# Optimization experiments

Hardware: AMD Instinct MI355X
Metric: run time of the kernel (lower is better)

## Reference

```python
import jax, jax.numpy as jnp
import numpy as np

B = 8192
LOD = 60      # latent_obs_dim
LSD = 2 * LOD # latent state dim
AD = 10       # act_dim
NB = 15       # num_basis
BW = 3        # bandwidth
H = 60        # control-net hidden units


def elup1(x):
    # exp(x) if x < 0 else x + 1 (positive covariance activation)
    return jnp.where(x < 0.0, jnp.exp(x), x + 1.0)


def setup_inputs() -> dict:
    key = jax.random.key(0)
    ks = jax.random.split(key, 16)
    inp = {
        "post_mean": jax.random.normal(ks[0], (B, LSD), jnp.float32),
        "cu": jax.random.uniform(ks[1], (B, LOD), jnp.float32) + 0.1,
        "cl": jax.random.uniform(ks[2], (B, LOD), jnp.float32) + 0.1,
        "cs": 0.01 * jax.random.normal(ks[3], (B, LOD), jnp.float32),
        "action": jax.random.normal(ks[4], (B, AD), jnp.float32),
        # transition basis matrices (params); original init is zeros/+-0.2*I,
        # use small random values for a non-degenerate numerical test
        "tm11": 0.05 * jax.random.normal(ks[5], (NB, LOD, LOD), jnp.float32),
        "tm12": 0.2 * jnp.eye(LOD)[None] + 0.02 * jax.random.normal(ks[6], (NB, LOD, LOD), jnp.float32),
        "tm21": -0.2 * jnp.eye(LOD)[None] + 0.02 * jax.random.normal(ks[7], (NB, LOD, LOD), jnp.float32),
        "tm22": 0.05 * jax.random.normal(ks[8], (NB, LOD, LOD), jnp.float32),
        # log transition noise, init elup1_inv(1.0) = 0.0 -> perturb slightly
        "log_noise": 0.1 * jax.random.normal(ks[9], (1, LSD), jnp.float32),
        # coefficient net: Linear(LSD -> NB) + Softmax (no hidden layers)
        "w_coef": jax.random.normal(ks[10], (NB, LSD), jnp.float32) / np.sqrt(LSD),
        "b_coef": jnp.zeros((NB,), jnp.float32),
        # control net: Linear(AD -> H) + ReLU + Linear(H -> LSD)
        "w_c1": jax.random.normal(ks[11], (H, AD), jnp.float32) / np.sqrt(AD),
        "b_c1": jnp.zeros((H,), jnp.float32),
        "w_c2": jax.random.normal(ks[12], (LSD, H), jnp.float32) / np.sqrt(H),
        "b_c2": jnp.zeros((LSD,), jnp.float32),
    }
    return inp


def _band_mask():
    idx = jnp.arange(LOD)
    return (jnp.abs(idx[:, None] - idx[None, :]) <= BW).astype(jnp.float32)


def reference(post_mean, cu, cl, cs, action,
              tm11, tm12, tm21, tm22, log_noise,
              w_coef, b_coef, w_c1, b_c1, w_c2, b_c2):
    mask = _band_mask()            # [LOD, LOD]
    eye = jnp.eye(LOD, dtype=post_mean.dtype)

    # coefficient net + softmax -> basis-weighted transition matrices
    coef = jax.nn.softmax(post_mean @ w_coef.T + b_coef, axis=-1)  # [B, NB]

    def mix(tm):  # [B, LOD, LOD], band-masked
        return jnp.einsum('bk,kij->bij', coef, tm) * mask

    t11 = mix(tm11) + eye
    t12 = mix(tm12)
    t21 = mix(tm21)
    t22 = mix(tm22) + eye

    # control net contribution
    control = jax.nn.relu(action @ w_c1.T + b_c1) @ w_c2.T + b_c2  # [B, LSD]

    trans_cov = elup1(log_noise)        # [1, LSD]
    tc_u = trans_cov[..., :LOD]
    tc_l = trans_cov[..., LOD:]

    mu = post_mean[:, :LOD]
    ml = post_mean[:, LOD:]

    bmv = lambda m, v: jnp.einsum('bij,bj->bi', m, v)

    nmu = bmv(t11, mu) + bmv(t12, ml)
    nml = bmv(t21, mu) + bmv(t22, ml)

    # diagonal covariance predict (dadat / dadbt)
    ncu = bmv(t11 ** 2, cu) + 2.0 * bmv(t11 * t12, cs) + bmv(t12 ** 2, cl) + tc_u
    ncl = bmv(t21 ** 2, cu) + 2.0 * bmv(t21 * t22, cs) + bmv(t22 ** 2, cl) + tc_l
    ncs = bmv(t21 * t11, cu) + bmv(t22 * t11, cs) + bmv(t21 * t12, cs) + bmv(t22 * t12, cl)

    next_mean = jnp.concatenate([nmu, nml], axis=-1) + control
    return (next_mean, ncu, ncl, ncs)
```

## Files before the change

### kernel.cpp

```cpp
#include <hip/hip_runtime.h>
#include <math.h>

#define BATCH 8192
#define LOD 60
#define LSD 120
#define AD 10
#define NB 15
#define BW 3
#define H 60

#define NM_SZ (BATCH * LSD)
#define NC_SZ (BATCH * LOD)

#define RGS 6
#define RG_ROWS 10
#define NJJ 16
#define VSJ 65
#define VSV (NJJ * VSJ)
#define VS_FLOATS (5 * VSV)
#define PACK_FLOATS (RG_ROWS * NB * 28)
#define OST_PLANE (RG_ROWS * 65)
#define OVL2 (VS_FLOATS + PACK_FLOATS)

__device__ __forceinline__ float elup1f(float x) {
    return x < 0.0f ? __expf(x) : x + 1.0f;
}

__global__ __launch_bounds__(256, 3) void k_fused(
    const float* __restrict__ pm, const float* __restrict__ cu,
    const float* __restrict__ cl, const float* __restrict__ cs,
    const float* __restrict__ action,
    const float* __restrict__ tm11, const float* __restrict__ tm12,
    const float* __restrict__ tm21, const float* __restrict__ tm22,
    const float* __restrict__ log_noise,
    const float* __restrict__ w_coef, const float* __restrict__ b_coef,
    const float* __restrict__ w_c1, const float* __restrict__ b_c1,
    const float* __restrict__ w_c2, const float* __restrict__ b_c2,
    float* __restrict__ out)
{
    __shared__ float coef_s[NB * 64];
    __shared__ __align__(16) float ovl[OVL2];

    const int tid  = threadIdx.x;
    const int wave = tid >> 6;
    const int lane = tid & 63;
    const int wv   = __builtin_amdgcn_readfirstlane(wave);

    const int bid  = blockIdx.x;
    const int xcd  = bid & 7;
    const int slot = bid >> 3;
    const int bg   = xcd * 16 + slot / RGS;
    const int rg   = slot % RGS;
    const int b0   = bg * 64;
    const int i0   = rg * RG_ROWS;

    {
        const int k0 = wv, k1 = wv + 4, k2 = wv + 8;
        const int k3 = (wv < 3) ? wv + 12 : 14;
        const float4* pmv = (const float4*)(pm + (size_t)(b0 + lane) * LSD);
        const float4* w0 = (const float4*)(w_coef + k0 * LSD);
        const float4* w1 = (const float4*)(w_coef + k1 * LSD);
        const float4* w2 = (const float4*)(w_coef + k2 * LSD);
        const float4* w3 = (const float4*)(w_coef + k3 * LSD);
        float a0 = b_coef[k0], a1 = b_coef[k1], a2 = b_coef[k2], a3 = b_coef[k3];
        #pragma unroll 6
        for (int d = 0; d < LSD / 4; ++d) {
            float4 p = pmv[d];
            float4 u0 = w0[d], u1 = w1[d], u2 = w2[d], u3 = w3[d];
            a0 = fmaf(p.x, u0.x, a0); a0 = fmaf(p.y, u0.y, a0);
            a0 = fmaf(p.z, u0.z, a0); a0 = fmaf(p.w, u0.w, a0);
            a1 = fmaf(p.x, u1.x, a1); a1 = fmaf(p.y, u1.y, a1);
            a1 = fmaf(p.z, u1.z, a1); a1 = fmaf(p.w, u1.w, a1);
            a2 = fmaf(p.x, u2.x, a2); a2 = fmaf(p.y, u2.y, a2);
            a2 = fmaf(p.z, u2.z, a2); a2 = fmaf(p.w, u2.w, a2);
            a3 = fmaf(p.x, u3.x, a3); a3 = fmaf(p.y, u3.y, a3);
            a3 = fmaf(p.z, u3.z, a3); a3 = fmaf(p.w, u3.w, a3);
        }
        coef_s[k0 * 64 + lane] = a0;
        coef_s[k1 * 64 + lane] = a1;
        coef_s[k2 * 64 + lane] = a2;
        if (wv < 3) coef_s[k3 * 64 + lane] = a3;
    }
    __syncthreads();

    float* vsb    = ovl;
    float* pack_s = ovl + VS_FLOATS;

    for (int idx = tid; idx < 5 * 64 * NJJ; idx += 256) {
        int jj  = idx & 15;
        int blc = (idx >> 4) & 63;
        int v   = idx >> 10;
        int j   = i0 - BW + jj;
        int bb  = b0 + blc;
        float val = 0.0f;
        if (j >= 0 && j < LOD) {
            if (v == 0)      val = pm[bb * LSD + j];
            else if (v == 1) val = pm[bb * LSD + LOD + j];
            else if (v == 2) val = cu[bb * LOD + j];
            else if (v == 3) val = cl[bb * LOD + j];
            else             val = cs[bb * LOD + j];
        }
        vsb[v * VSV + jj * VSJ + blc] = val;
    }
    for (int idx = tid; idx < PACK_FLOATS; idx += 256) {
        int m  = idx & 3;
        int q  = idx >> 2;
        int jo = q % 7;
        int q2 = q / 7;
        int k  = q2 % NB;
        int ri = q2 / NB;
        int i  = i0 + ri;
        int j  = i - BW + jo;
        const float* tmm = (m == 0) ? tm11 : (m == 1) ? tm12 : (m == 2) ? tm21 : tm22;
        float val = (j >= 0 && j < LOD) ? tmm[k * (LOD * LOD) + i * LOD + j] : 0.0f;
        pack_s[idx] = val;
    }

    if (tid < 64) {
        float v[NB];
        float mx = -1e30f;
        #pragma unroll
        for (int k = 0; k < NB; ++k) { v[k] = coef_s[k * 64 + tid]; mx = fmaxf(mx, v[k]); }
        float sm = 0.0f;
        #pragma unroll
        for (int k = 0; k < NB; ++k) { v[k] = __expf(v[k] - mx); sm += v[k]; }
        float inv = 1.0f / sm;
        #pragma unroll
        for (int k = 0; k < NB; ++k) coef_s[k * 64 + tid] = v[k] * inv;
    }

    const int lim   = (wv < 2) ? 2 : 1;
    const int rbase = (wv < 2) ? wv * 3 : 6 + (wv - 2) * 2;
    int rcl[3];
    rcl[0] = rbase; rcl[1] = rbase + 1; rcl[2] = rbase + lim;

    float ctl[6];
    #pragma unroll
    for (int rr = 0; rr < 3; ++rr) {
        ctl[rr]     = b_c2[i0 + rcl[rr]];
        ctl[3 + rr] = b_c2[LOD + i0 + rcl[rr]];
    }
    {
        float av[AD];
        const float2* a2p = (const float2*)(action + (size_t)(b0 + lane) * AD);
        #pragma unroll
        for (int z = 0; z < 5; ++z) { float2 t2 = a2p[z]; av[2 * z] = t2.x; av[2 * z + 1] = t2.y; }
        #pragma unroll 4
        for (int h = 0; h < H; ++h) {
            float hv = b_c1[h];
            #pragma unroll
            for (int a = 0; a < AD; ++a) hv = fmaf(av[a], w_c1[h * AD + a], hv);
            hv = fmaxf(hv, 0.0f);
            #pragma unroll
            for (int rr = 0; rr < 3; ++rr) {
                ctl[rr]     = fmaf(hv, w_c2[(i0 + rcl[rr]) * H + h], ctl[rr]);
                ctl[3 + rr] = fmaf(hv, w_c2[(LOD + i0 + rcl[rr]) * H + h], ctl[3 + rr]);
            }
        }
    }
    __syncthreads();

    float cf[NB];
    #pragma unroll
    for (int k = 0; k < NB; ++k) cf[k] = coef_s[k * 64 + lane];

    float onm[3], onl[3], ouv[3], olv[3], osv[3];
    #pragma unroll
    for (int rr = 0; rr < 3; ++rr) {
        const int riu = rcl[rr];
        const int iu  = i0 + riu;

        float t[28];
        #pragma unroll
        for (int z = 0; z < 28; ++z) t[z] = 0.0f;
        const float4* tp = (const float4*)pack_s + riu * (NB * 7);
        #pragma unroll
        for (int k = 0; k < NB; ++k) {
            float c = cf[k];
            #pragma unroll
            for (int jo = 0; jo < 7; ++jo) {
                float4 tv = tp[k * 7 + jo];
                t[jo * 4 + 0] = fmaf(c, tv.x, t[jo * 4 + 0]);
                t[jo * 4 + 1] = fmaf(c, tv.y, t[jo * 4 + 1]);
                t[jo * 4 + 2] = fmaf(c, tv.z, t[jo * 4 + 2]);
                t[jo * 4 + 3] = fmaf(c, tv.w, t[jo * 4 + 3]);
            }
        }
        t[3 * 4 + 0] += 1.0f;
        t[3 * 4 + 3] += 1.0f;

        float nmu = 0.f, nml = 0.f, ncuv = 0.f, nclv = 0.f, ncsv = 0.f;
        #pragma unroll
        for (int jo = 0; jo < 7; ++jo) {
            const int jj = riu + jo;
            float m_ = vsb[0 * VSV + jj * VSJ + lane];
            float n_ = vsb[1 * VSV + jj * VSJ + lane];
            float u_ = vsb[2 * VSV + jj * VSJ + lane];
            float l_ = vsb[3 * VSV + jj * VSJ + lane];
            float s_ = vsb[4 * VSV + jj * VSJ + lane];
            float A = t[jo * 4 + 0], Bv = t[jo * 4 + 1];
            float C = t[jo * 4 + 2], D  = t[jo * 4 + 3];
            nmu = fmaf(A, m_, nmu);  nmu = fmaf(Bv, n_, nmu);
            nml = fmaf(C, m_, nml);  nml = fmaf(D, n_, nml);
            float e1 = fmaf(Bv, s_, A * u_);
            float e2 = fmaf(Bv, l_, A * s_);
            float f1 = fmaf(D, s_, C * u_);
            float f2 = fmaf(D, l_, C * s_);
            ncuv = fmaf(A, e1, ncuv);  ncuv = fmaf(Bv, e2, ncuv);
            nclv = fmaf(C, f1, nclv);  nclv = fmaf(D, f2, nclv);
            ncsv = fmaf(C, e1, ncsv);  ncsv = fmaf(D, e2, ncsv);
        }
        ncuv += elup1f(log_noise[iu]);
        nclv += elup1f(log_noise[LOD + iu]);
        nmu  += ctl[rr];
        nml  += ctl[3 + rr];
        onm[rr] = nmu; onl[rr] = nml; ouv[rr] = ncuv; olv[rr] = nclv; osv[rr] = ncsv;
    }
    __syncthreads();

    float* ost = ovl + VS_FLOATS;
    #pragma unroll
    for (int rr = 0; rr < 3; ++rr) {
        const int ri = rcl[rr];
        ost[0 * OST_PLANE + ri * 65 + lane] = onm[rr];
        ost[1 * OST_PLANE + ri * 65 + lane] = onl[rr];
        ost[2 * OST_PLANE + ri * 65 + lane] = ouv[rr];
        ost[3 * OST_PLANE + ri * 65 + lane] = olv[rr];
        ost[4 * OST_PLANE + ri * 65 + lane] = osv[rr];
    }
    __syncthreads();

    for (int idx = tid; idx < 5 * 64 * 16; idx += 256) {
        int rq  = idx & 15;
        if (rq >= RG_ROWS) continue;
        int blc = (idx >> 4) & 63;
        int t5  = idx >> 10;
        int bb  = b0 + blc;
        float v = ost[t5 * OST_PLANE + rq * 65 + blc];
        float* bp;
        if (t5 == 0)      bp = out + bb * LSD + i0;
        else if (t5 == 1) bp = out + bb * LSD + LOD + i0;
        else if (t5 == 2) bp = out + NM_SZ + bb * LOD + i0;
        else if (t5 == 3) bp = out + NM_SZ + NC_SZ + bb * LOD + i0;
        else              bp = out + NM_SZ + 2 * NC_SZ + bb * LOD + i0;
        bp[rq] = v;
    }
}

extern "C" void kernel_launch(void* const* d_in, const int* in_sizes, int n_in,
                              void* d_out, int out_size, void* d_ws, size_t ws_size,
                              hipStream_t stream) {
    (void)in_sizes; (void)n_in; (void)out_size; (void)d_ws; (void)ws_size;
    const float* pm        = (const float*)d_in[0];
    const float* cu        = (const float*)d_in[1];
    const float* cl        = (const float*)d_in[2];
    const float* cs        = (const float*)d_in[3];
    const float* action    = (const float*)d_in[4];
    const float* tm11      = (const float*)d_in[5];
    const float* tm12      = (const float*)d_in[6];
    const float* tm21      = (const float*)d_in[7];
    const float* tm22      = (const float*)d_in[8];
    const float* log_noise = (const float*)d_in[9];
    const float* w_coef    = (const float*)d_in[10];
    const float* b_coef    = (const float*)d_in[11];
    const float* w_c1      = (const float*)d_in[12];
    const float* b_c1      = (const float*)d_in[13];
    const float* w_c2      = (const float*)d_in[14];
    const float* b_c2      = (const float*)d_in[15];

    hipLaunchKernelGGL(k_fused, dim3(768), dim3(256), 0, stream,
                       pm, cu, cl, cs, action, tm11, tm12, tm21, tm22,
                       log_noise, w_coef, b_coef, w_c1, b_c1, w_c2, b_c2,
                       (float*)d_out);
}
```

Measured before the change: 131.4 us.

## Repartition row groups to 8x8, split control MLP across waves, vectorize stores

Splits the 60 output rows into 8 groups of 8 rows, with the last group padded and clamped, and launches 1024 blocks with a 4-blocks-per-CU launch bound. The control net's hidden layer is now computed once per block, split across waves into shared memory, so it is no longer recomputed per wave. The band vector loads are prefetched into registers before the shared-memory write, and softmax is done per wave rather than by a single wave. Outputs are written as float4 stores. The aim is better load balance and overlap; the cost is padded rows in the last group, extra redundant recomputation of coefficients in each of the 1024 blocks, and added register pressure under the tighter launch bound.

Result: faster. 119.2 us (-9.3%).

```diff
diff --git a/kernel.cpp b/kernel.cpp
--- a/kernel.cpp
+++ b/kernel.cpp
@@ -12,21 +12,24 @@
 #define NM_SZ (BATCH * LSD)
 #define NC_SZ (BATCH * LOD)
 
-#define RGS 6
-#define RG_ROWS 10
+#define RGS 8
+#define RG_ROWS 8
 #define NJJ 16
 #define VSJ 65
 #define VSV (NJJ * VSJ)
+#define PACK_FLOATS (RG_ROWS * NB * 28)
+#define VS_OFF PACK_FLOATS
 #define VS_FLOATS (5 * VSV)
-#define PACK_FLOATS (RG_ROWS * NB * 28)
+#define OVL_FLOATS (VS_OFF + VS_FLOATS)
+#define COEF_OFF VS_OFF
+#define HID_OFF (VS_OFF + NB * 64)
 #define OST_PLANE (RG_ROWS * 65)
-#define OVL2 (VS_FLOATS + PACK_FLOATS)
 
 __device__ __forceinline__ float elup1f(float x) {
     return x < 0.0f ? __expf(x) : x + 1.0f;
 }
 
-__global__ __launch_bounds__(256, 3) void k_fused(
+__global__ __launch_bounds__(256, 4) void k_fused(
     const float* __restrict__ pm, const float* __restrict__ cu,
     const float* __restrict__ cl, const float* __restrict__ cs,
     const float* __restrict__ action,
@@ -38,21 +41,24 @@
     const float* __restrict__ w_c2, const float* __restrict__ b_c2,
     float* __restrict__ out)
 {
-    __shared__ float coef_s[NB * 64];
-    __shared__ __align__(16) float ovl[OVL2];
+    __shared__ __align__(16) float ovl[OVL_FLOATS];
 
     const int tid  = threadIdx.x;
-    const int wave = tid >> 6;
     const int lane = tid & 63;
-    const int wv   = __builtin_amdgcn_readfirstlane(wave);
+    const int wv   = __builtin_amdgcn_readfirstlane(tid >> 6);
 
     const int bid  = blockIdx.x;
     const int xcd  = bid & 7;
     const int slot = bid >> 3;
-    const int bg   = xcd * 16 + slot / RGS;
-    const int rg   = slot % RGS;
+    const int bg   = xcd * 16 + (slot >> 3);
+    const int rg   = slot & 7;
     const int b0   = bg * 64;
     const int i0   = rg * RG_ROWS;
+
+    float* pack_s = ovl;
+    float* vsb    = ovl + VS_OFF;
+    float* coefL  = ovl + COEF_OFF;
+    float* hid_s  = ovl + HID_OFF;
 
     {
         const int k0 = wv, k1 = wv + 4, k2 = wv + 8;
@@ -76,32 +82,51 @@
             a3 = fmaf(p.x, u3.x, a3); a3 = fmaf(p.y, u3.y, a3);
             a3 = fmaf(p.z, u3.z, a3); a3 = fmaf(p.w, u3.w, a3);
         }
-        coef_s[k0 * 64 + lane] = a0;
-        coef_s[k1 * 64 + lane] = a1;
-        coef_s[k2 * 64 + lane] = a2;
-        if (wv < 3) coef_s[k3 * 64 + lane] = a3;
-    }
-    __syncthreads();
-
-    float* vsb    = ovl;
-    float* pack_s = ovl + VS_FLOATS;
-
-    for (int idx = tid; idx < 5 * 64 * NJJ; idx += 256) {
-        int jj  = idx & 15;
-        int blc = (idx >> 4) & 63;
-        int v   = idx >> 10;
-        int j   = i0 - BW + jj;
-        int bb  = b0 + blc;
-        float val = 0.0f;
-        if (j >= 0 && j < LOD) {
-            if (v == 0)      val = pm[bb * LSD + j];
-            else if (v == 1) val = pm[bb * LSD + LOD + j];
-            else if (v == 2) val = cu[bb * LOD + j];
-            else if (v == 3) val = cl[bb * LOD + j];
-            else             val = cs[bb * LOD + j];
-        }
-        vsb[v * VSV + jj * VSJ + blc] = val;
-    }
+        coefL[k0 * 64 + lane] = a0;
+        coefL[k1 * 64 + lane] = a1;
+        coefL[k2 * 64 + lane] = a2;
+        if (wv < 3) coefL[k3 * 64 + lane] = a3;
+    }
+    {
+        float av[AD];
+        const float2* a2p = (const float2*)(action + (size_t)(b0 + lane) * AD);
+        #pragma unroll
+        for (int z = 0; z < 5; ++z) { float2 t2 = a2p[z]; av[2 * z] = t2.x; av[2 * z + 1] = t2.y; }
+        #pragma unroll
+        for (int q = 0; q < 15; ++q) {
+            int h = wv * 15 + q;
+            float acc = b_c1[h];
+            #pragma unroll
+            for (int a = 0; a < AD; ++a)
+                acc = fmaf(av[a], w_c1[h * AD + a], acc);
+            hid_s[h * 65 + lane] = fmaxf(acc, 0.0f);
+        }
+    }
+    __syncthreads();
+
+    float vr[20];
+    {
+        const int jj  = tid & 15;
+        const int j   = i0 - BW + jj;
+        const bool jok = (j >= 0) && (j < LOD);
+        #pragma unroll
+        for (int z = 0; z < 20; ++z) {
+            const int idx = z * 256 + tid;
+            const int blc = (idx >> 4) & 63;
+            const int bb  = b0 + blc;
+            float val = 0.0f;
+            if (jok) {
+                const int v = z >> 2;
+                if (v == 0)      val = pm[bb * LSD + j];
+                else if (v == 1) val = pm[bb * LSD + LOD + j];
+                else if (v == 2) val = cu[bb * LOD + j];
+                else if (v == 3) val = cl[bb * LOD + j];
+                else             val = cs[bb * LOD + j];
+            }
+            vr[z] = val;
+        }
+    }
+
     for (int idx = tid; idx < PACK_FLOATS; idx += 256) {
         int m  = idx & 3;
         int q  = idx >> 2;
@@ -112,63 +137,55 @@
         int i  = i0 + ri;
         int j  = i - BW + jo;
         const float* tmm = (m == 0) ? tm11 : (m == 1) ? tm12 : (m == 2) ? tm21 : tm22;
-        float val = (j >= 0 && j < LOD) ? tmm[k * (LOD * LOD) + i * LOD + j] : 0.0f;
+        float val = (i < LOD && j >= 0 && j < LOD) ? tmm[k * (LOD * LOD) + i * LOD + j] : 0.0f;
         pack_s[idx] = val;
     }
 
-    if (tid < 64) {
-        float v[NB];
+    float cf[NB];
+    {
         float mx = -1e30f;
         #pragma unroll
-        for (int k = 0; k < NB; ++k) { v[k] = coef_s[k * 64 + tid]; mx = fmaxf(mx, v[k]); }
+        for (int k = 0; k < NB; ++k) { cf[k] = coefL[k * 64 + lane]; mx = fmaxf(mx, cf[k]); }
         float sm = 0.0f;
         #pragma unroll
-        for (int k = 0; k < NB; ++k) { v[k] = __expf(v[k] - mx); sm += v[k]; }
+        for (int k = 0; k < NB; ++k) { cf[k] = __expf(cf[k] - mx); sm += cf[k]; }
         float inv = 1.0f / sm;
         #pragma unroll
-        for (int k = 0; k < NB; ++k) coef_s[k * 64 + tid] = v[k] * inv;
-    }
-
-    const int lim   = (wv < 2) ? 2 : 1;
-    const int rbase = (wv < 2) ? wv * 3 : 6 + (wv - 2) * 2;
-    int rcl[3];
-    rcl[0] = rbase; rcl[1] = rbase + 1; rcl[2] = rbase + lim;
-
-    float ctl[6];
+        for (int k = 0; k < NB; ++k) cf[k] *= inv;
+    }
+
+    const int r0g = i0 + 2 * wv;
+    const int c0  = (r0g < LOD) ? r0g : LOD - 1;
+    const int c1  = (r0g + 1 < LOD) ? r0g + 1 : LOD - 1;
+    float ctl0 = b_c2[c0], ctl1 = b_c2[c1];
+    float ctl2 = b_c2[LOD + c0], ctl3 = b_c2[LOD + c1];
+    #pragma unroll 4
+    for (int h = 0; h < H; ++h) {
+        float hv = hid_s[h * 65 + lane];
+        ctl0 = fmaf(hv, w_c2[c0 * H + h], ctl0);
+        ctl1 = fmaf(hv, w_c2[c1 * H + h], ctl1);
+        ctl2 = fmaf(hv, w_c2[(LOD + c0) * H + h], ctl2);
+        ctl3 = fmaf(hv, w_c2[(LOD + c1) * H + h], ctl3);
+    }
+    __syncthreads();
+
+    {
+        const int jj = tid & 15;
+        #pragma unroll
+        for (int z = 0; z < 20; ++z) {
+            const int idx = z * 256 + tid;
+            const int blc = (idx >> 4) & 63;
+            vsb[(z >> 2) * VSV + jj * VSJ + blc] = vr[z];
+        }
+    }
+    __syncthreads();
+
+    float onm[2], onl[2], ouv[2], olv[2], osv[2];
     #pragma unroll
-    for (int rr = 0; rr < 3; ++rr) {
-        ctl[rr]     = b_c2[i0 + rcl[rr]];
-        ctl[3 + rr] = b_c2[LOD + i0 + rcl[rr]];
-    }
-    {
-        float av[AD];
-        const float2* a2p = (const float2*)(action + (size_t)(b0 + lane) * AD);
-        #pragma unroll
-        for (int z = 0; z < 5; ++z) { float2 t2 = a2p[z]; av[2 * z] = t2.x; av[2 * z + 1] = t2.y; }
-        #pragma unroll 4
-        for (int h = 0; h < H; ++h) {
-            float hv = b_c1[h];
-            #pragma unroll
-            for (int a = 0; a < AD; ++a) hv = fmaf(av[a], w_c1[h * AD + a], hv);
-            hv = fmaxf(hv, 0.0f);
-            #pragma unroll
-            for (int rr = 0; rr < 3; ++rr) {
-                ctl[rr]     = fmaf(hv, w_c2[(i0 + rcl[rr]) * H + h], ctl[rr]);
-                ctl[3 + rr] = fmaf(hv, w_c2[(LOD + i0 + rcl[rr]) * H + h], ctl[3 + rr]);
-            }
-        }
-    }
-    __syncthreads();
-
-    float cf[NB];
-    #pragma unroll
-    for (int k = 0; k < NB; ++k) cf[k] = coef_s[k * 64 + lane];
-
-    float onm[3], onl[3], ouv[3], olv[3], osv[3];
-    #pragma unroll
-    for (int rr = 0; rr < 3; ++rr) {
-        const int riu = rcl[rr];
+    for (int rr = 0; rr < 2; ++rr) {
+        const int riu = 2 * wv + rr;
         const int iu  = i0 + riu;
+        const int iuc = (iu < LOD) ? iu : LOD - 1;
 
         float t[28];
         #pragma unroll
@@ -210,18 +227,18 @@
             nclv = fmaf(C, f1, nclv);  nclv = fmaf(D, f2, nclv);
             ncsv = fmaf(C, e1, ncsv);  ncsv = fmaf(D, e2, ncsv);
         }
-        ncuv += elup1f(log_noise[iu]);
-        nclv += elup1f(log_noise[LOD + iu]);
-        nmu  += ctl[rr];
-        nml  += ctl[3 + rr];
+        ncuv += elup1f(log_noise[iuc]);
+        nclv += elup1f(log_noise[LOD + iuc]);
+        nmu  += (rr == 0) ? ctl0 : ctl1;
+        nml  += (rr == 0) ? ctl2 : ctl3;
         onm[rr] = nmu; onl[rr] = nml; ouv[rr] = ncuv; olv[rr] = nclv; osv[rr] = ncsv;
     }
     __syncthreads();
 
-    float* ost = ovl + VS_FLOATS;
+    float* ost = ovl;
     #pragma unroll
-    for (int rr = 0; rr < 3; ++rr) {
-        const int ri = rcl[rr];
+    for (int rr = 0; rr < 2; ++rr) {
+        const int ri = 2 * wv + rr;
         ost[0 * OST_PLANE + ri * 65 + lane] = onm[rr];
         ost[1 * OST_PLANE + ri * 65 + lane] = onl[rr];
         ost[2 * OST_PLANE + ri * 65 + lane] = ouv[rr];
@@ -230,20 +247,25 @@
     }
     __syncthreads();
 
-    for (int idx = tid; idx < 5 * 64 * 16; idx += 256) {
-        int rq  = idx & 15;
-        if (rq >= RG_ROWS) continue;
-        int blc = (idx >> 4) & 63;
-        int t5  = idx >> 10;
-        int bb  = b0 + blc;
-        float v = ost[t5 * OST_PLANE + rq * 65 + blc];
+    for (int idx = tid; idx < 5 * 64 * 2; idx += 256) {
+        int q   = idx & 1;
+        int blc = (idx >> 1) & 63;
+        int t5  = idx >> 7;
+        if (i0 + q * 4 + 3 >= LOD) continue;
+        int bb = b0 + blc;
+        int ro = q * 4;
+        float4 v;
+        v.x = ost[t5 * OST_PLANE + (ro + 0) * 65 + blc];
+        v.y = ost[t5 * OST_PLANE + (ro + 1) * 65 + blc];
+        v.z = ost[t5 * OST_PLANE + (ro + 2) * 65 + blc];
+        v.w = ost[t5 * OST_PLANE + (ro + 3) * 65 + blc];
         float* bp;
         if (t5 == 0)      bp = out + bb * LSD + i0;
         else if (t5 == 1) bp = out + bb * LSD + LOD + i0;
         else if (t5 == 2) bp = out + NM_SZ + bb * LOD + i0;
         else if (t5 == 3) bp = out + NM_SZ + NC_SZ + bb * LOD + i0;
         else              bp = out + NM_SZ + 2 * NC_SZ + bb * LOD + i0;
-        bp[rq] = v;
+        *(float4*)(bp + ro) = v;
     }
 }
 
@@ -268,7 +290,7 @@
     const float* w_c2      = (const float*)d_in[14];
     const float* b_c2      = (const float*)d_in[15];
 
-    hipLaunchKernelGGL(k_fused, dim3(768), dim3(256), 0, stream,
+    hipLaunchKernelGGL(k_fused, dim3(1024), dim3(256), 0, stream,
                        pm, cu, cl, cs, action, tm11, tm12, tm21, tm22,
                        log_noise, w_coef, b_coef, w_c1, b_c1, w_c2, b_c2,
                        (float*)d_out);
```
